# Performance work log

Measured on AMD Instinct MI355X. Metric: run time of the kernel, lower is better.

The kernel has to match this reference:

```python
import jax, jax.numpy as jnp
import numpy as np

B, PQ, C, NH, L, P, FF = 8, 900, 256, 8, 4, 4, 2048
SHAPES = [(100, 152), (50, 76), (25, 38), (13, 19)]
PK = sum(h * w for h, w in SHAPES)
DH = C // NH


def setup_inputs() -> dict:
    key = jax.random.key(0)
    ks = jax.random.split(key, 20)
    s = 0.02
    w = lambda i, shp: jax.random.normal(ks[i], shp, jnp.float32) * s
    starts = np.cumsum([0] + [h * wd for h, wd in SHAPES[:-1]]).astype(np.int64)
    return dict(
        query=w(0, (B, C, PQ)),
        key=w(1, (B, C, PK)),
        query_pos=jax.random.uniform(ks[2], (B, PQ, 3)),
        key_pos=jax.random.uniform(ks[3], (B, PK, 3)),
        reference_points=jax.random.uniform(ks[4], (B, PQ, L, 2)),
        W_in=w(5, (3 * C, C)), b_in=jnp.zeros(3 * C),
        W_out=w(6, (C, C)), b_out=jnp.zeros(C),
        W_off=w(7, (NH * L * P * 2, C)),
        b_off=jax.random.uniform(ks[8], (NH * L * P * 2,), minval=-1.0, maxval=1.0),
        W_aw=w(9, (NH * L * P, C)), b_aw=jnp.zeros(NH * L * P),
        W_v=w(10, (C, C)), b_v=jnp.zeros(C),
        W_o=w(11, (C, C)), b_o=jnp.zeros(C),
        W1=w(12, (FF, C)), b1=jnp.zeros(FF),
        W2=w(13, (C, FF)), b2=jnp.zeros(C),
        g1=jnp.ones(C), be1=jnp.zeros(C),
        g2=jnp.ones(C), be2=jnp.zeros(C),
        g3=jnp.ones(C), be3=jnp.zeros(C),
        spatial_shapes=np.array(SHAPES, np.int64),
        level_start_index=starts,
    )


def layer_norm(x, g, b):
    m = x.mean(-1, keepdims=True)
    v = x.var(-1, keepdims=True)
    return (x - m) * jax.lax.rsqrt(v + 1e-5) * g + b


def mha(x, W_in, b_in, W_out, b_out):
    # x: [S, B, C]; torch nn.MultiheadAttention with q=k=v=x
    S, Bn, _ = x.shape
    qkv = x @ W_in.T + b_in
    q, k, v = jnp.split(qkv, 3, axis=-1)
    to_h = lambda t: t.reshape(S, Bn, NH, DH).transpose(1, 2, 0, 3)  # [B,H,S,Dh]
    q, k, v = to_h(q), to_h(k), to_h(v)
    attn = jax.nn.softmax(jnp.einsum('bhqd,bhkd->bhqk', q, k) / np.sqrt(DH), axis=-1)
    o = jnp.einsum('bhqk,bhkd->bhqd', attn, v).transpose(2, 0, 1, 3).reshape(S, Bn, C)
    return o @ W_out.T + b_out


def ms_deform(value, loc, aw, shapes, starts):
    # value [B,PK,NH,DH], loc [B,PQ,NH,L,P,2] in [0,1], aw [B,PQ,NH,L,P]
    v = value.transpose(0, 2, 1, 3)          # [B,NH,PK,DH]
    locT = loc.transpose(0, 2, 1, 3, 4, 5)   # [B,NH,PQ,L,P,2]
    awT = aw.transpose(0, 2, 1, 3, 4)        # [B,NH,PQ,L,P]
    out = jnp.zeros((B, NH, PQ, DH), value.dtype)
    for l, (Hl, Wl) in enumerate(shapes):
        st = starts[l]
        vl = v[:, :, st:st + Hl * Wl]        # [B,NH,Hl*Wl,DH]
        x = locT[..., l, :, 0] * Wl - 0.5    # [B,NH,PQ,P]  (align_corners=False)
        y = locT[..., l, :, 1] * Hl - 0.5
        x0 = jnp.floor(x); y0 = jnp.floor(y)
        lw, lh = x - x0, y - y0
        x0i = x0.astype(jnp.int32); y0i = y0.astype(jnp.int32)

        def gather(ix, iy):
            valid = ((ix >= 0) & (ix < Wl) & (iy >= 0) & (iy < Hl)).astype(vl.dtype)
            idx = jnp.clip(iy, 0, Hl - 1) * Wl + jnp.clip(ix, 0, Wl - 1)
            g = jnp.take_along_axis(vl, idx.reshape(B, NH, -1, 1), axis=2)
            return g.reshape(B, NH, PQ, P, DH) * valid[..., None]

        samp = (gather(x0i, y0i) * ((1 - lw) * (1 - lh))[..., None]
                + gather(x0i + 1, y0i) * (lw * (1 - lh))[..., None]
                + gather(x0i, y0i + 1) * ((1 - lw) * lh)[..., None]
                + gather(x0i + 1, y0i + 1) * (lw * lh)[..., None])  # [B,NH,PQ,P,DH]
        out = out + (samp * awT[..., l, :, None]).sum(3)
    return out.transpose(0, 2, 1, 3).reshape(B, PQ, C)


def reference(query, key, query_pos, key_pos, reference_points,
              W_in, b_in, W_out, b_out, W_off, b_off, W_aw, b_aw,
              W_v, b_v, W_o, b_o, W1, b1, W2, b2,
              g1, be1, g2, be2, g3, be3,
              spatial_shapes, level_start_index):
    shapes = [tuple(int(t) for t in r) for r in np.asarray(spatial_shapes)]
    starts = [int(t) for t in np.asarray(level_start_index)]
    q = query.transpose(2, 0, 1)   # [PQ,B,C]
    k = key.transpose(2, 0, 1)     # [PK,B,C]
    # self-attention (posembeds are None in this config)
    q = layer_norm(q + mha(q, W_in, b_in, W_out, b_out), g1, be1)
    # multi-scale deformable cross-attention
    qd = q.transpose(1, 0, 2)      # [B,PQ,C]
    kf = k.transpose(1, 0, 2)      # [B,PK,C]
    value = (kf @ W_v.T + b_v).reshape(B, PK, NH, DH)
    off = (qd @ W_off.T + b_off).reshape(B, PQ, NH, L, P, 2)
    aw = jax.nn.softmax((qd @ W_aw.T + b_aw).reshape(B, PQ, NH, L * P), -1)
    aw = aw.reshape(B, PQ, NH, L, P)
    norm = jnp.asarray([[w_, h_] for (h_, w_) in shapes], jnp.float32)  # [L,2] as (W,H)
    loc = reference_points[:, :, None, :, None, :] + off / norm[None, None, None, :, None, :]
    q2 = ms_deform(value, loc, aw, shapes, starts) @ W_o.T + b_o
    q = layer_norm(q + q2.transpose(1, 0, 2), g2, be2)
    # FFN
    ff = jax.nn.relu(q @ W1.T + b1) @ W2.T + b2
    q = layer_norm(q + ff, g3, be3)
    return q.transpose(1, 2, 0)    # [B,C,PQ]
```

## Files before the change

kernel.cpp:

```cpp
#include <hip/hip_runtime.h>
#include <hip/hip_bf16.h>
#include <stdint.h>

typedef __hip_bfloat16 bf16;
typedef short bf16x8 __attribute__((ext_vector_type(8)));
typedef short s4v    __attribute__((ext_vector_type(4)));
typedef float f32x4  __attribute__((ext_vector_type(4)));

constexpr int B_  = 8;
constexpr int PQ_ = 900;
constexpr int C_  = 256;
constexpr int NH_ = 8;
constexpr int L_  = 4;
constexpr int P_  = 4;
constexpr int FF_ = 2048;
constexpr int DH_ = 32;
constexpr int PK_ = 20197;
constexpr int VLD = 960;

__device__ __forceinline__ short f2b(float f) {
    __hip_bfloat16 h = __float2bfloat16(f);
    union { __hip_bfloat16 h; short s; } u; u.h = h; return u.s;
}
__device__ __forceinline__ float b2f(short s) {
    union { short s; __hip_bfloat16 h; } u; u.s = s; return __bfloat162float(u.h);
}

__launch_bounds__(256)
__global__ void wcvt_kernel(const float* __restrict__ p0, const float* __restrict__ p1,
                            const float* __restrict__ p2, const float* __restrict__ p3,
                            const float* __restrict__ p4, const float* __restrict__ p5,
                            const float* __restrict__ p6, const float* __restrict__ p7,
                            short* __restrict__ dst)
{
    const int g = (blockIdx.x * 256 + threadIdx.x) * 4;
    const float* src; int off;
    if      (g < 196608)  { src = p0; off = 0; }
    else if (g < 262144)  { src = p1; off = 196608; }
    else if (g < 327680)  { src = p2; off = 262144; }
    else if (g < 360448)  { src = p3; off = 327680; }
    else if (g < 425984)  { src = p4; off = 360448; }
    else if (g < 491520)  { src = p5; off = 425984; }
    else if (g < 1015808) { src = p6; off = 491520; }
    else                  { src = p7; off = 1015808; }
    float4 v = *(const float4*)(src + (g - off));
    s4v pk = {f2b(v.x), f2b(v.y), f2b(v.z), f2b(v.w)};
    *(s4v*)&dst[g] = pk;
}

template <int NF, bool DBUF, bool AF32, bool WF32, bool CF32, bool RELU>
__launch_bounds__(256)
__global__ void mfma_gemm(const void* __restrict__ Ap, const void* __restrict__ Wp,
                          const float* __restrict__ bias, void* __restrict__ Cp,
                          int Mb, int N, int K, int tilesM,
                          int ldA, int ldW, int ldC, int nbI,
                          int64_t sAo, int64_t sAi, int64_t sWo, int64_t sWi,
                          int64_t sCo, int64_t sCi, float scale)
{
    constexpr int BN  = 64 * NF;
    constexpr int LDR = 72;
    constexpr int NB  = DBUF ? 2 : 1;
    __shared__ short As[NB * 64 * LDR];
    __shared__ short Ws[NB * BN * LDR];

    const int tid   = threadIdx.x;
    const int batch = blockIdx.y / tilesM;
    const int m0    = (blockIdx.y % tilesM) * 64;
    const int n0    = blockIdx.x * BN;
    const int outer = batch / nbI, inner = batch % nbI;
    const int64_t offA = (int64_t)outer * sAo + (int64_t)inner * sAi;
    const int64_t offW = (int64_t)outer * sWo + (int64_t)inner * sWi;
    const int64_t offC = (int64_t)outer * sCo + (int64_t)inner * sCi;

    const int w = tid >> 6, lane = tid & 63;
    const int quad = lane >> 4, lrow = lane & 15;
    const int colbase = n0 + w * 16 * NF;

    const int sm  = tid >> 2;
    const int skb = (tid & 3) * 16;

    const int T = (K + 63) / 64;

    bf16x8 areg[2];
    bf16x8 wreg[2 * NF];

    auto stageA = [&](int t) {
        const int k0 = t * 64;
        const int gm = m0 + sm;
#pragma unroll
        for (int c = 0; c < 2; ++c) {
            const int k = k0 + skb + c * 8;
            bf16x8 pk = {0, 0, 0, 0, 0, 0, 0, 0};
            if (gm < Mb && k + 8 <= K) {
                if (AF32) {
                    const float* s = (const float*)Ap + offA + (int64_t)gm * ldA + k;
                    float4 u0 = *(const float4*)s;
                    float4 u1 = *(const float4*)(s + 4);
                    pk = (bf16x8){f2b(u0.x), f2b(u0.y), f2b(u0.z), f2b(u0.w),
                                  f2b(u1.x), f2b(u1.y), f2b(u1.z), f2b(u1.w)};
                } else {
                    pk = *(const bf16x8*)((const short*)Ap + offA + (int64_t)gm * ldA + k);
                }
            }
            areg[c] = pk;
        }
    };
    auto stageW = [&](int t) {
        const int k0 = t * 64;
#pragma unroll
        for (int j = 0; j < NF; ++j) {
            const int gn = n0 + j * 64 + sm;
#pragma unroll
            for (int c = 0; c < 2; ++c) {
                const int k = k0 + skb + c * 8;
                bf16x8 pk = {0, 0, 0, 0, 0, 0, 0, 0};
                if (gn < N && k + 8 <= K) {
                    if (WF32) {
                        const float* s = (const float*)Wp + offW + (int64_t)gn * ldW + k;
                        float4 u0 = *(const float4*)s;
                        float4 u1 = *(const float4*)(s + 4);
                        pk = (bf16x8){f2b(u0.x), f2b(u0.y), f2b(u0.z), f2b(u0.w),
                                      f2b(u1.x), f2b(u1.y), f2b(u1.z), f2b(u1.w)};
                    } else {
                        pk = *(const bf16x8*)((const short*)Wp + offW + (int64_t)gn * ldW + k);
                    }
                }
                wreg[j * 2 + c] = pk;
            }
        }
    };
    auto writeLDS = [&](int buf) {
#pragma unroll
        for (int c = 0; c < 2; ++c)
            *(bf16x8*)&As[(buf * 64 + sm) * LDR + skb + c * 8] = areg[c];
#pragma unroll
        for (int j = 0; j < NF; ++j)
#pragma unroll
            for (int c = 0; c < 2; ++c)
                *(bf16x8*)&Ws[(buf * BN + j * 64 + sm) * LDR + skb + c * 8] = wreg[j * 2 + c];
    };

    f32x4 acc[4][NF];
#pragma unroll
    for (int i = 0; i < 4; ++i)
#pragma unroll
        for (int j = 0; j < NF; ++j) acc[i][j] = (f32x4){0.f, 0.f, 0.f, 0.f};

    auto compute = [&](int buf) {
        bf16x8 a[4][2], bb[NF][2];
#pragma unroll
        for (int kh = 0; kh < 2; ++kh) {
#pragma unroll
            for (int mf = 0; mf < 4; ++mf)
                a[mf][kh] = *(const bf16x8*)&As[(buf * 64 + mf * 16 + lrow) * LDR + kh * 32 + quad * 8];
#pragma unroll
            for (int nf = 0; nf < NF; ++nf)
                bb[nf][kh] = *(const bf16x8*)&Ws[(buf * BN + w * 16 * NF + nf * 16 + lrow) * LDR + kh * 32 + quad * 8];
        }
#pragma unroll
        for (int kh = 0; kh < 2; ++kh)
#pragma unroll
            for (int mf = 0; mf < 4; ++mf)
#pragma unroll
                for (int nf = 0; nf < NF; ++nf)
                    acc[mf][nf] = __builtin_amdgcn_mfma_f32_16x16x32_bf16(a[mf][kh], bb[nf][kh], acc[mf][nf], 0, 0, 0);
    };

    if (DBUF) {
        stageA(0); stageW(0); writeLDS(0);
        __syncthreads();
        for (int t = 0; t < T; ++t) {
            const int cur = t & 1;
            if (t + 1 < T) { stageA(t + 1); stageW(t + 1); }
            compute(cur);
            if (t + 1 < T) {
                writeLDS(cur ^ 1);
                __syncthreads();
            }
        }
    } else {
        for (int t = 0; t < T; ++t) {
            stageA(t); stageW(t);
            if (t > 0) __syncthreads();
            writeLDS(0);
            __syncthreads();
            compute(0);
        }
    }

#pragma unroll
    for (int nf = 0; nf < NF; ++nf) {
        const int col = colbase + nf * 16 + lrow;
        if (col >= N) continue;
        const float bia = bias ? bias[col] : 0.f;
#pragma unroll
        for (int mf = 0; mf < 4; ++mf) {
            const int row0 = m0 + mf * 16 + quad * 4;
#pragma unroll
            for (int r = 0; r < 4; ++r) {
                const int rr = row0 + r;
                if (rr < Mb) {
                    float v = acc[mf][nf][r] * scale + bia;
                    if (RELU) v = fmaxf(v, 0.f);
                    const int64_t idx = offC + (int64_t)rr * ldC + col;
                    if (CF32) ((float*)Cp)[idx] = v;
                    else      ((short*)Cp)[idx] = f2b(v);
                }
            }
        }
    }
}

template <int NF, bool DBUF, bool AF32, bool WF32, bool CF32, bool RELU>
static void mfma_launch(const void* A, const void* W, const float* bias, void* Cp,
                        int nb, int nbI, int Mb, int N, int K,
                        int ldA, int ldW, int ldC,
                        int64_t sAo, int64_t sAi, int64_t sWo, int64_t sWi,
                        int64_t sCo, int64_t sCi, float scale, hipStream_t stream)
{
    int tilesM = (Mb + 63) / 64;
    dim3 grid((N + 64 * NF - 1) / (64 * NF), nb * tilesM);
    mfma_gemm<NF, DBUF, AF32, WF32, CF32, RELU><<<grid, 256, 0, stream>>>(
        A, W, bias, Cp, Mb, N, K, tilesM, ldA, ldW, ldC, nbI,
        sAo, sAi, sWo, sWi, sCo, sCi, scale);
}

__launch_bounds__(256)
__global__ void vproj_kernel(const short* __restrict__ A, const short* __restrict__ Wb,
                             const float* __restrict__ bias, short* __restrict__ Cp,
                             int Mb, int nTiles)
{
    __shared__ short Ws[128 * 256];
    const int tid = threadIdx.x;
    const int n0 = blockIdx.x * 128;
    const int w = tid >> 6, lane = tid & 63;
    const int quad = lane >> 4, lrow = lane & 15;

    {
        const int n = tid >> 1, hk = tid & 1;
        const int64_t src = (int64_t)(n0 + n) * 256 + hk * 128;
#pragma unroll
        for (int j = 0; j < 16; ++j) {
            const int slot = hk * 16 + j;
            bf16x8 pk = *(const bf16x8*)&Wb[src + j * 8];
            *(bf16x8*)((char*)Ws + n * 512 + ((slot ^ (n & 7)) << 4)) = pk;
        }
    }
    __syncthreads();

    const int nbase = w * 32;
    float bia[2];
#pragma unroll
    for (int nf = 0; nf < 2; ++nf) bia[nf] = bias[n0 + nbase + nf * 16 + lrow];

    for (int it = 0; it < 4; ++it) {
        const int ti = blockIdx.y * 4 + it;
        if (ti >= nTiles) break;
        const int m0 = ti * 64;

        f32x4 acc[4][2];
#pragma unroll
        for (int mf = 0; mf < 4; ++mf)
#pragma unroll
            for (int nf = 0; nf < 2; ++nf) acc[mf][nf] = (f32x4){0.f, 0.f, 0.f, 0.f};

#pragma unroll
        for (int kh = 0; kh < 8; ++kh) {
            bf16x8 a[4];
#pragma unroll
            for (int mf = 0; mf < 4; ++mf) {
                const int gm = m0 + mf * 16 + lrow;
                a[mf] = (gm < Mb)
                    ? *(const bf16x8*)&A[(int64_t)gm * 256 + kh * 32 + quad * 8]
                    : (bf16x8){0, 0, 0, 0, 0, 0, 0, 0};
            }
            bf16x8 b[2];
#pragma unroll
            for (int nf = 0; nf < 2; ++nf) {
                const int n = nbase + nf * 16 + lrow;
                b[nf] = *(const bf16x8*)((const char*)Ws + n * 512 +
                                         ((((kh << 2) | quad) ^ (lrow & 7)) << 4));
            }
#pragma unroll
            for (int mf = 0; mf < 4; ++mf)
#pragma unroll
                for (int nf = 0; nf < 2; ++nf)
                    acc[mf][nf] = __builtin_amdgcn_mfma_f32_16x16x32_bf16(a[mf], b[nf], acc[mf][nf], 0, 0, 0);
        }

#pragma unroll
        for (int nf = 0; nf < 2; ++nf) {
            const int col = n0 + nbase + nf * 16 + lrow;
#pragma unroll
            for (int mf = 0; mf < 4; ++mf) {
#pragma unroll
                for (int r = 0; r < 4; ++r) {
                    const int rr = m0 + mf * 16 + quad * 4 + r;
                    if (rr < Mb)
                        Cp[(int64_t)rr * 256 + col] = f2b(acc[mf][nf][r] + bia[nf]);
                }
            }
        }
    }
}

__launch_bounds__(256)
__global__ void transpose_kernel(const float* __restrict__ src, short* __restrict__ dst,
                                 int Scount, int ldS, int64_t sbs, int64_t dbs)
{
    const int tid = threadIdx.x;
    const int b = blockIdx.z;
    const int s0 = blockIdx.x * 32, c0 = blockIdx.y * 32;
    __shared__ float t[32][33];
    {
        const int c_l = tid >> 3, sq = (tid & 7) * 4;
        const int64_t base = (int64_t)b * sbs + (int64_t)(c0 + c_l) * ldS;
#pragma unroll
        for (int i = 0; i < 4; ++i) {
            const int s = s0 + sq + i;
            t[c_l][sq + i] = (s < Scount) ? src[base + s] : 0.f;
        }
    }
    __syncthreads();
    {
        const int s_l = tid >> 3, cq = (tid & 7) * 4;
        const int s = s0 + s_l;
        if (s < Scount) {
            s4v pk = {f2b(t[cq + 0][s_l]), f2b(t[cq + 1][s_l]),
                      f2b(t[cq + 2][s_l]), f2b(t[cq + 3][s_l])};
            *(s4v*)&dst[(int64_t)b * dbs + (int64_t)s * 256 + c0 + cq] = pk;
        }
    }
}

__launch_bounds__(256)
__global__ void vt_kernel(const short* __restrict__ qkv, short* __restrict__ VT)
{
    const int tid = threadIdx.x;
    const int bh = blockIdx.y, b = bh >> 3, h = bh & 7;
    const int s0 = blockIdx.x * 32;
    __shared__ short t[32][36];
    {
        const int s_l = tid >> 3, dq = (tid & 7) * 4;
        const int s = s0 + s_l;
        s4v pk = {0, 0, 0, 0};
        if (s < 900)
            pk = *(const s4v*)&qkv[((int64_t)(b * 900 + s)) * 768 + 512 + h * 32 + dq];
        *(s4v*)&t[s_l][dq] = pk;
    }
    __syncthreads();
    {
        const int d = tid >> 3, sq = (tid & 7) * 4;
        s4v pk = {t[sq + 0][d], t[sq + 1][d], t[sq + 2][d], t[sq + 3][d]};
        *(s4v*)&VT[((int64_t)bh * 32 + d) * VLD + s0 + sq] = pk;
    }
}

__launch_bounds__(256)
__global__ void attn_fused(const short* __restrict__ qkv, const short* __restrict__ VT,
                           short* __restrict__ attno)
{
    __shared__ short Pl[4 * 16 * 72];
    const int tid = threadIdx.x;
    const int wv = tid >> 6, lane = tid & 63;
    const int quad = lane >> 4, lrow = lane & 15;
    const int bh = blockIdx.y, b = bh >> 3, h = bh & 7;
    const int q0 = blockIdx.x * 64 + wv * 16;
    const float iscale = 0.17677669529663687f;

    bf16x8 aq = {0, 0, 0, 0, 0, 0, 0, 0};
    {
        const int q = q0 + lrow;
        if (q < 900)
            aq = *(const bf16x8*)&qkv[((int64_t)(b * 900 + q)) * 768 + h * 32 + quad * 8];
    }

    float mrow[4], lsum[4];
    f32x4 o[2] = {{0.f, 0.f, 0.f, 0.f}, {0.f, 0.f, 0.f, 0.f}};
#pragma unroll
    for (int r = 0; r < 4; ++r) { mrow[r] = -1e30f; lsum[r] = 0.f; }

    short* Pw = &Pl[wv * 16 * 72];

    for (int st = 0; st < 15; ++st) {
        const int s0 = st * 64;
        f32x4 sc[4];
#pragma unroll
        for (int nf = 0; nf < 4; ++nf) {
            const int s = s0 + nf * 16 + lrow;
            bf16x8 kb = {0, 0, 0, 0, 0, 0, 0, 0};
            if (s < 900)
                kb = *(const bf16x8*)&qkv[((int64_t)(b * 900 + s)) * 768 + 256 + h * 32 + quad * 8];
            sc[nf] = __builtin_amdgcn_mfma_f32_16x16x32_bf16(aq, kb, (f32x4){0.f, 0.f, 0.f, 0.f}, 0, 0, 0);
        }
#pragma unroll
        for (int nf = 0; nf < 4; ++nf) {
            const int s = s0 + nf * 16 + lrow;
            if (s >= 900) sc[nf] = (f32x4){-1e30f, -1e30f, -1e30f, -1e30f};
            else {
#pragma unroll
                for (int r = 0; r < 4; ++r) sc[nf][r] *= iscale;
            }
        }
        float alpha[4], ps[4][4], rsum[4];
#pragma unroll
        for (int r = 0; r < 4; ++r) {
            float tm = fmaxf(fmaxf(sc[0][r], sc[1][r]), fmaxf(sc[2][r], sc[3][r]));
#pragma unroll
            for (int off = 1; off < 16; off <<= 1)
                tm = fmaxf(tm, __shfl_xor(tm, off, 64));
            const float nm = fmaxf(mrow[r], tm);
            alpha[r] = __expf(mrow[r] - nm);
            mrow[r] = nm;
            float s4 = 0.f;
#pragma unroll
            for (int nf = 0; nf < 4; ++nf) {
                const float p = __expf(sc[nf][r] - nm);
                ps[nf][r] = p;
                s4 += p;
            }
#pragma unroll
            for (int off = 1; off < 16; off <<= 1)
                s4 += __shfl_xor(s4, off, 64);
            rsum[r] = s4;
        }
#pragma unroll
        for (int nf2 = 0; nf2 < 2; ++nf2)
#pragma unroll
            for (int r = 0; r < 4; ++r) o[nf2][r] *= alpha[r];
#pragma unroll
        for (int r = 0; r < 4; ++r) lsum[r] = lsum[r] * alpha[r] + rsum[r];
#pragma unroll
        for (int nf = 0; nf < 4; ++nf)
#pragma unroll
            for (int r = 0; r < 4; ++r)
                Pw[(quad * 4 + r) * 72 + nf * 16 + lrow] = f2b(ps[nf][r]);
#pragma unroll
        for (int kh = 0; kh < 2; ++kh) {
            bf16x8 pa = *(const bf16x8*)&Pw[lrow * 72 + kh * 32 + quad * 8];
#pragma unroll
            for (int nf2 = 0; nf2 < 2; ++nf2) {
                const int d = nf2 * 16 + lrow;
                bf16x8 vb = *(const bf16x8*)&VT[((int64_t)bh * 32 + d) * VLD + s0 + kh * 32 + quad * 8];
                o[nf2] = __builtin_amdgcn_mfma_f32_16x16x32_bf16(pa, vb, o[nf2], 0, 0, 0);
            }
        }
    }
#pragma unroll
    for (int r = 0; r < 4; ++r) {
        const int q = q0 + quad * 4 + r;
        if (q < 900) {
            const float inv = 1.f / lsum[r];
#pragma unroll
            for (int nf2 = 0; nf2 < 2; ++nf2)
                attno[((int64_t)(b * 900 + q)) * 256 + h * 32 + nf2 * 16 + lrow] = f2b(o[nf2][r] * inv);
        }
    }
}

template <int MODE>
__launch_bounds__(256)
__global__ void ln_kernel(const float* __restrict__ y, const void* __restrict__ res,
                          const float* __restrict__ g, const float* __restrict__ be,
                          float* __restrict__ out_f, short* __restrict__ out_b)
{
    const int bt = blockIdx.x;
    const int b = bt / PQ_, t = bt % PQ_;
    const int c = threadIdx.x;

    float r;
    if (MODE == 0)      r = ((const float*)res)[((int64_t)b * C_ + c) * PQ_ + t];
    else if (MODE == 1) r = ((const float*)res)[(int64_t)bt * C_ + c];
    else                r = b2f(((const short*)res)[(int64_t)bt * C_ + c]);
    const float v = r + y[(int64_t)bt * C_ + c];

    __shared__ float s1[256], s2[256];
    s1[c] = v; s2[c] = v * v;
    __syncthreads();
    for (int st = 128; st > 0; st >>= 1) {
        if (c < st) { s1[c] += s1[c + st]; s2[c] += s2[c + st]; }
        __syncthreads();
    }
    const float mean = s1[0] * (1.f / C_);
    const float var  = s2[0] * (1.f / C_) - mean * mean;
    const float o = (v - mean) * rsqrtf(var + 1e-5f) * g[c] + be[c];

    if (MODE == 0) { out_f[(int64_t)bt * C_ + c] = o; out_b[(int64_t)bt * C_ + c] = f2b(o); }
    else if (MODE == 1) out_b[(int64_t)bt * C_ + c] = f2b(o);
    else out_f[((int64_t)b * C_ + c) * PQ_ + t] = o;
}

__launch_bounds__(256)
__global__ void deform_kernel(const float* __restrict__ offb, const float* __restrict__ awl,
                              const float* __restrict__ refp, const short* __restrict__ value,
                              short* __restrict__ samp)
{
    const int bt = blockIdx.x;
    const int b = bt / PQ_;
    const int tid = threadIdx.x;
    const int h = tid >> 5, d = tid & 31;

    __shared__ float Loff[256];
    __shared__ float Law[128];
    __shared__ float Lref[8];

    Loff[tid] = offb[(int64_t)bt * 256 + tid];
    if (tid < 128) Law[tid] = awl[(int64_t)bt * 128 + tid];
    if (tid < 8)   Lref[tid] = refp[(int64_t)bt * 8 + tid];
    __syncthreads();

    float m = -1e30f;
#pragma unroll
    for (int i = 0; i < 16; ++i) m = fmaxf(m, Law[h * 16 + i]);
    float s = 0.f;
#pragma unroll
    for (int i = 0; i < 16; ++i) s += __expf(Law[h * 16 + i] - m);
    const float invs = 1.f / s;

    const int HLc[4] = {100, 50, 25, 13};
    const int WLc[4] = {152, 76, 38, 19};
    const int STc[4] = {0, 15200, 19000, 19950};

    float acc = 0.f;
#pragma unroll
    for (int l = 0; l < L_; ++l) {
        const int Hl = HLc[l], Wl = WLc[l], st0 = STc[l];
        const float fx = Lref[l * 2 + 0], fy = Lref[l * 2 + 1];
#pragma unroll
        for (int p = 0; p < P_; ++p) {
            const float ox = Loff[h * 32 + l * 8 + p * 2 + 0];
            const float oy = Loff[h * 32 + l * 8 + p * 2 + 1];
            const float x = (fx + ox / (float)Wl) * (float)Wl - 0.5f;
            const float y = (fy + oy / (float)Hl) * (float)Hl - 0.5f;
            const float x0f = floorf(x), y0f = floorf(y);
            const int x0 = (int)x0f, y0 = (int)y0f;
            const float lw = x - x0f, lh = y - y0f;
            const float w00 = (1.f - lw) * (1.f - lh), w10 = lw * (1.f - lh);
            const float w01 = (1.f - lw) * lh,         w11 = lw * lh;
            const float aww = __expf(Law[h * 16 + l * 4 + p] - m) * invs;

            float sv = 0.f;
            int ix, iy; float w;
#pragma unroll
            for (int cidx = 0; cidx < 4; ++cidx) {
                if (cidx == 0) { ix = x0;     iy = y0;     w = w00; }
                if (cidx == 1) { ix = x0 + 1; iy = y0;     w = w10; }
                if (cidx == 2) { ix = x0;     iy = y0 + 1; w = w01; }
                if (cidx == 3) { ix = x0 + 1; iy = y0 + 1; w = w11; }
                if (ix >= 0 && ix < Wl && iy >= 0 && iy < Hl) {
                    const int64_t vi = ((int64_t)(b * PK_ + st0 + iy * Wl + ix)) * 256 + h * 32 + d;
                    sv += w * b2f(value[vi]);
                }
            }
            acc += sv * aww;
        }
    }
    samp[(int64_t)bt * 256 + tid] = f2b(acc);
}

extern "C" void kernel_launch(void* const* d_in, const int* in_sizes, int n_in,
                              void* d_out, int out_size, void* d_ws, size_t ws_size,
                              hipStream_t stream)
{
    const float* query = (const float*)d_in[0];
    const float* key   = (const float*)d_in[1];
    const float* refp  = (const float*)d_in[4];
    const float* W_in  = (const float*)d_in[5];
    const float* b_in  = (const float*)d_in[6];
    const float* W_out = (const float*)d_in[7];
    const float* b_out = (const float*)d_in[8];
    const float* W_off = (const float*)d_in[9];
    const float* b_off = (const float*)d_in[10];
    const float* W_aw  = (const float*)d_in[11];
    const float* b_aw  = (const float*)d_in[12];
    const float* W_v   = (const float*)d_in[13];
    const float* b_v   = (const float*)d_in[14];
    const float* W_o   = (const float*)d_in[15];
    const float* b_o   = (const float*)d_in[16];
    const float* W1    = (const float*)d_in[17];
    const float* b1    = (const float*)d_in[18];
    const float* W2    = (const float*)d_in[19];
    const float* b2    = (const float*)d_in[20];
    const float* g1    = (const float*)d_in[21];
    const float* be1   = (const float*)d_in[22];
    const float* g2    = (const float*)d_in[23];
    const float* be2   = (const float*)d_in[24];
    const float* g3    = (const float*)d_in[25];
    const float* be3   = (const float*)d_in[26];

    char* X  = (char*)d_ws;
    char* Yb = X + 62259200;
    char* Z1 = Yb + 7372800;
    char* Wa = Z1 + 7372800;
    char* Wb_ = Wa + 3686400;
    char* KT = Wb_ + 3686400;
    char* VA = KT + 82726912;
    char* WB = VA + 82726912;

    short* qkvb   = (short*)X;
    short* queryT = (short*)(X + 11059200);
    short* VT     = (short*)(X + 14745600);
    short* attno  = (short*)(X + 18677760);
    short* ffh    = (short*)X;
    float* proj   = (float*)Yb;
    float* offb   = (float*)Yb;
    float* proj2  = (float*)Yb;
    float* ffo    = (float*)Yb;
    float* q1     = (float*)Z1;
    short* q1b    = (short*)Wa;
    short* samp   = (short*)Wa;
    float* awl    = (float*)Wb_;
    short* q2nb   = (short*)Wb_;
    short* keyT   = (short*)KT;
    short* value  = (short*)VA;

    short* WBs    = (short*)WB;
    short* Wb_in  = WBs;
    short* Wb_out = WBs + 196608;
    short* Wb_off = WBs + 262144;
    short* Wb_aw  = WBs + 327680;
    short* Wb_v   = WBs + 360448;
    short* Wb_o   = WBs + 425984;
    short* Wb1    = WBs + 491520;
    short* Wb2    = WBs + 1015808;

    wcvt_kernel<<<1504, 256, 0, stream>>>(W_in, W_out, W_off, W_aw, W_v, W_o, W1, W2, WBs);
    transpose_kernel<<<dim3(29, 8, B_), 256, 0, stream>>>(query, queryT, PQ_, PQ_,
                                                          (int64_t)C_ * PQ_, (int64_t)PQ_ * C_);
    mfma_launch<1, true, false, false, false, false>(queryT, Wb_in, b_in, qkvb, 1, 1, B_ * PQ_, 768, 256,
                                                     256, 256, 768, 0, 0, 0, 0, 0, 0, 1.f, stream);
    vt_kernel<<<dim3(30, 64), 256, 0, stream>>>(qkvb, VT);
    attn_fused<<<dim3(15, 64), 256, 0, stream>>>(qkvb, VT, attno);
    mfma_launch<1, true, false, false, true, false>(attno, Wb_out, b_out, proj, 1, 1, B_ * PQ_, 256, 256,
                                                    256, 256, 256, 0, 0, 0, 0, 0, 0, 1.f, stream);
    ln_kernel<0><<<B_ * PQ_, 256, 0, stream>>>(proj, query, g1, be1, q1, q1b);
    mfma_launch<1, true, false, false, true, false>(q1b, Wb_off, b_off, offb, 1, 1, B_ * PQ_, 256, 256,
                                                    256, 256, 256, 0, 0, 0, 0, 0, 0, 1.f, stream);
    mfma_launch<1, true, false, false, true, false>(q1b, Wb_aw, b_aw, awl, 1, 1, B_ * PQ_, 128, 256,
                                                    256, 256, 128, 0, 0, 0, 0, 0, 0, 1.f, stream);
    transpose_kernel<<<dim3((PK_ + 31) / 32, 8, B_), 256, 0, stream>>>(
        key, keyT, PK_, PK_, (int64_t)C_ * PK_, (int64_t)PK_ * 256);
    {
        const int nTiles = (B_ * PK_ + 63) / 64;
        vproj_kernel<<<dim3(2, (nTiles + 3) / 4), 256, 0, stream>>>(
            keyT, Wb_v, b_v, value, B_ * PK_, nTiles);
    }
    deform_kernel<<<B_ * PQ_, 256, 0, stream>>>(offb, awl, refp, value, samp);
    mfma_launch<1, true, false, false, true, false>(samp, Wb_o, b_o, proj2, 1, 1, B_ * PQ_, 256, 256,
                                                    256, 256, 256, 0, 0, 0, 0, 0, 0, 1.f, stream);
    ln_kernel<1><<<B_ * PQ_, 256, 0, stream>>>(proj2, q1, g2, be2, nullptr, q2nb);
    mfma_launch<1, true, false, false, false, true>(q2nb, Wb1, b1, ffh, 1, 1, B_ * PQ_, FF_, 256,
                                                    256, 256, FF_, 0, 0, 0, 0, 0, 0, 1.f, stream);
    mfma_launch<1, true, false, false, true, false>(ffh, Wb2, b2, ffo, 1, 1, B_ * PQ_, 256, FF_,
                                                    FF_, FF_, 256, 0, 0, 0, 0, 0, 0, 1.f, stream);
    ln_kernel<2><<<B_ * PQ_, 256, 0, stream>>>(ffo, q2nb, g3, be3, (float*)d_out, nullptr);

    (void)in_sizes; (void)n_in; (void)out_size; (void)ws_size;
}
```

Baseline: 739.2 us.

## Hold weight tiles in registers for K=256 GEMMs and use wave-shuffle LayerNorm

Adds a GEMM kernel that loads each wave's 32-column slice of the full K=256 weight into registers once, then streams four 64-row A tiles straight from global memory into MFMA. It replaces the shared-memory vproj kernel and the generic double-buffered mfma_gemm for every K=256 projection (QKV, out-proj, offsets, attention weights, value, W_o, FFN1). The goal is to drop LDS staging and barriers and to reuse weights across row tiles. LayerNorm's tree reduction in shared memory becomes a wave shuffle reduction with a single barrier. The trade-offs are higher register pressure and uncoalesced, unstaged A loads from global memory.

```diff
diff --git a/kernel.cpp b/kernel.cpp
--- a/kernel.cpp
+++ b/kernel.cpp
@@ -46,6 +46,85 @@
     float4 v = *(const float4*)(src + (g - off));
     s4v pk = {f2b(v.x), f2b(v.y), f2b(v.z), f2b(v.w)};
     *(s4v*)&dst[g] = pk;
+}
+
+template <bool CF32, bool RELU>
+__launch_bounds__(256)
+__global__ void wreg_gemm(const short* __restrict__ A, const short* __restrict__ Wb,
+                          const float* __restrict__ bias, void* __restrict__ Cp,
+                          int Mb, int nTiles, int ldC)
+{
+    const int tid = threadIdx.x;
+    const int w = tid >> 6, lane = tid & 63;
+    const int quad = lane >> 4, lrow = lane & 15;
+    const int nbase = blockIdx.x * 128 + w * 32;
+
+    bf16x8 wreg[8][2];
+#pragma unroll
+    for (int kh = 0; kh < 8; ++kh)
+#pragma unroll
+        for (int nf = 0; nf < 2; ++nf)
+            wreg[kh][nf] = *(const bf16x8*)&Wb[(int64_t)(nbase + nf * 16 + lrow) * 256 + kh * 32 + quad * 8];
+
+    float bia[2];
+#pragma unroll
+    for (int nf = 0; nf < 2; ++nf) bia[nf] = bias ? bias[nbase + nf * 16 + lrow] : 0.f;
+
+    for (int it = 0; it < 4; ++it) {
+        const int ti = blockIdx.y * 4 + it;
+        if (ti >= nTiles) break;
+        const int m0 = ti * 64;
+
+        f32x4 acc[4][2];
+#pragma unroll
+        for (int mf = 0; mf < 4; ++mf)
+#pragma unroll
+            for (int nf = 0; nf < 2; ++nf) acc[mf][nf] = (f32x4){0.f, 0.f, 0.f, 0.f};
+
+#pragma unroll
+        for (int kh = 0; kh < 8; ++kh) {
+            bf16x8 a[4];
+#pragma unroll
+            for (int mf = 0; mf < 4; ++mf) {
+                const int gm = m0 + mf * 16 + lrow;
+                a[mf] = (gm < Mb)
+                    ? *(const bf16x8*)&A[(int64_t)gm * 256 + kh * 32 + quad * 8]
+                    : (bf16x8){0, 0, 0, 0, 0, 0, 0, 0};
+            }
+#pragma unroll
+            for (int mf = 0; mf < 4; ++mf)
+#pragma unroll
+                for (int nf = 0; nf < 2; ++nf)
+                    acc[mf][nf] = __builtin_amdgcn_mfma_f32_16x16x32_bf16(a[mf], wreg[kh][nf], acc[mf][nf], 0, 0, 0);
+        }
+
+#pragma unroll
+        for (int nf = 0; nf < 2; ++nf) {
+            const int col = nbase + nf * 16 + lrow;
+#pragma unroll
+            for (int mf = 0; mf < 4; ++mf) {
+#pragma unroll
+                for (int r = 0; r < 4; ++r) {
+                    const int rr = m0 + mf * 16 + quad * 4 + r;
+                    if (rr < Mb) {
+                        float v = acc[mf][nf][r] + bia[nf];
+                        if (RELU) v = fmaxf(v, 0.f);
+                        if (CF32) ((float*)Cp)[(int64_t)rr * ldC + col] = v;
+                        else      ((short*)Cp)[(int64_t)rr * ldC + col] = f2b(v);
+                    }
+                }
+            }
+        }
+    }
+}
+
+template <bool CF32, bool RELU>
+static void wreg_launch(const short* A, const short* Wb, const float* bias, void* Cp,
+                        int Mb, int N, int ldC, hipStream_t stream)
+{
+    const int nTiles = (Mb + 63) / 64;
+    dim3 grid(N / 128, (nTiles + 3) / 4);
+    wreg_gemm<CF32, RELU><<<grid, 256, 0, stream>>>(A, Wb, bias, Cp, Mb, nTiles, ldC);
 }
 
 template <int NF, bool DBUF, bool AF32, bool WF32, bool CF32, bool RELU>
@@ -226,85 +305,6 @@
 }
 
 __launch_bounds__(256)
-__global__ void vproj_kernel(const short* __restrict__ A, const short* __restrict__ Wb,
-                             const float* __restrict__ bias, short* __restrict__ Cp,
-                             int Mb, int nTiles)
-{
-    __shared__ short Ws[128 * 256];
-    const int tid = threadIdx.x;
-    const int n0 = blockIdx.x * 128;
-    const int w = tid >> 6, lane = tid & 63;
-    const int quad = lane >> 4, lrow = lane & 15;
-
-    {
-        const int n = tid >> 1, hk = tid & 1;
-        const int64_t src = (int64_t)(n0 + n) * 256 + hk * 128;
-#pragma unroll
-        for (int j = 0; j < 16; ++j) {
-            const int slot = hk * 16 + j;
-            bf16x8 pk = *(const bf16x8*)&Wb[src + j * 8];
-            *(bf16x8*)((char*)Ws + n * 512 + ((slot ^ (n & 7)) << 4)) = pk;
-        }
-    }
-    __syncthreads();
-
-    const int nbase = w * 32;
-    float bia[2];
-#pragma unroll
-    for (int nf = 0; nf < 2; ++nf) bia[nf] = bias[n0 + nbase + nf * 16 + lrow];
-
-    for (int it = 0; it < 4; ++it) {
-        const int ti = blockIdx.y * 4 + it;
-        if (ti >= nTiles) break;
-        const int m0 = ti * 64;
-
-        f32x4 acc[4][2];
-#pragma unroll
-        for (int mf = 0; mf < 4; ++mf)
-#pragma unroll
-            for (int nf = 0; nf < 2; ++nf) acc[mf][nf] = (f32x4){0.f, 0.f, 0.f, 0.f};
-
-#pragma unroll
-        for (int kh = 0; kh < 8; ++kh) {
-            bf16x8 a[4];
-#pragma unroll
-            for (int mf = 0; mf < 4; ++mf) {
-                const int gm = m0 + mf * 16 + lrow;
-                a[mf] = (gm < Mb)
-                    ? *(const bf16x8*)&A[(int64_t)gm * 256 + kh * 32 + quad * 8]
-                    : (bf16x8){0, 0, 0, 0, 0, 0, 0, 0};
-            }
-            bf16x8 b[2];
-#pragma unroll
-            for (int nf = 0; nf < 2; ++nf) {
-                const int n = nbase + nf * 16 + lrow;
-                b[nf] = *(const bf16x8*)((const char*)Ws + n * 512 +
-                                         ((((kh << 2) | quad) ^ (lrow & 7)) << 4));
-            }
-#pragma unroll
-            for (int mf = 0; mf < 4; ++mf)
-#pragma unroll
-                for (int nf = 0; nf < 2; ++nf)
-                    acc[mf][nf] = __builtin_amdgcn_mfma_f32_16x16x32_bf16(a[mf], b[nf], acc[mf][nf], 0, 0, 0);
-        }
-
-#pragma unroll
-        for (int nf = 0; nf < 2; ++nf) {
-            const int col = n0 + nbase + nf * 16 + lrow;
-#pragma unroll
-            for (int mf = 0; mf < 4; ++mf) {
-#pragma unroll
-                for (int r = 0; r < 4; ++r) {
-                    const int rr = m0 + mf * 16 + quad * 4 + r;
-                    if (rr < Mb)
-                        Cp[(int64_t)rr * 256 + col] = f2b(acc[mf][nf][r] + bia[nf]);
-                }
-            }
-        }
-    }
-}
-
-__launch_bounds__(256)
 __global__ void transpose_kernel(const float* __restrict__ src, short* __restrict__ dst,
                                  int Scount, int ldS, int64_t sbs, int64_t dbs)
 {
@@ -467,6 +467,7 @@
     const int bt = blockIdx.x;
     const int b = bt / PQ_, t = bt % PQ_;
     const int c = threadIdx.x;
+    const int wv = c >> 6, lane = c & 63;
 
     float r;
     if (MODE == 0)      r = ((const float*)res)[((int64_t)b * C_ + c) * PQ_ + t];
@@ -474,15 +475,19 @@
     else                r = b2f(((const short*)res)[(int64_t)bt * C_ + c]);
     const float v = r + y[(int64_t)bt * C_ + c];
 
-    __shared__ float s1[256], s2[256];
-    s1[c] = v; s2[c] = v * v;
+    __shared__ float p1[4], p2[4];
+    float a = v, sq = v * v;
+#pragma unroll
+    for (int off = 32; off > 0; off >>= 1) {
+        a  += __shfl_xor(a, off, 64);
+        sq += __shfl_xor(sq, off, 64);
+    }
+    if (lane == 0) { p1[wv] = a; p2[wv] = sq; }
     __syncthreads();
-    for (int st = 128; st > 0; st >>= 1) {
-        if (c < st) { s1[c] += s1[c + st]; s2[c] += s2[c + st]; }
-        __syncthreads();
-    }
-    const float mean = s1[0] * (1.f / C_);
-    const float var  = s2[0] * (1.f / C_) - mean * mean;
+    const float s1 = p1[0] + p1[1] + p1[2] + p1[3];
+    const float s2 = p2[0] + p2[1] + p2[2] + p2[3];
+    const float mean = s1 * (1.f / C_);
+    const float var  = s2 * (1.f / C_) - mean * mean;
     const float o = (v - mean) * rsqrtf(var + 1e-5f) * g[c] + be[c];
 
     if (MODE == 0) { out_f[(int64_t)bt * C_ + c] = o; out_b[(int64_t)bt * C_ + c] = f2b(o); }
@@ -627,30 +632,20 @@
     wcvt_kernel<<<1504, 256, 0, stream>>>(W_in, W_out, W_off, W_aw, W_v, W_o, W1, W2, WBs);
     transpose_kernel<<<dim3(29, 8, B_), 256, 0, stream>>>(query, queryT, PQ_, PQ_,
                                                           (int64_t)C_ * PQ_, (int64_t)PQ_ * C_);
-    mfma_launch<1, true, false, false, false, false>(queryT, Wb_in, b_in, qkvb, 1, 1, B_ * PQ_, 768, 256,
-                                                     256, 256, 768, 0, 0, 0, 0, 0, 0, 1.f, stream);
+    wreg_launch<false, false>(queryT, Wb_in, b_in, qkvb, B_ * PQ_, 768, 768, stream);
     vt_kernel<<<dim3(30, 64), 256, 0, stream>>>(qkvb, VT);
     attn_fused<<<dim3(15, 64), 256, 0, stream>>>(qkvb, VT, attno);
-    mfma_launch<1, true, false, false, true, false>(attno, Wb_out, b_out, proj, 1, 1, B_ * PQ_, 256, 256,
-                                                    256, 256, 256, 0, 0, 0, 0, 0, 0, 1.f, stream);
+    wreg_launch<true, false>(attno, Wb_out, b_out, proj, B_ * PQ_, 256, 256, stream);
     ln_kernel<0><<<B_ * PQ_, 256, 0, stream>>>(proj, query, g1, be1, q1, q1b);
-    mfma_launch<1, true, false, false, true, false>(q1b, Wb_off, b_off, offb, 1, 1, B_ * PQ_, 256, 256,
-                                                    256, 256, 256, 0, 0, 0, 0, 0, 0, 1.f, stream);
-    mfma_launch<1, true, false, false, true, false>(q1b, Wb_aw, b_aw, awl, 1, 1, B_ * PQ_, 128, 256,
-                                                    256, 256, 128, 0, 0, 0, 0, 0, 0, 1.f, stream);
+    wreg_launch<true, false>(q1b, Wb_off, b_off, offb, B_ * PQ_, 256, 256, stream);
+    wreg_launch<true, false>(q1b, Wb_aw, b_aw, awl, B_ * PQ_, 128, 128, stream);
     transpose_kernel<<<dim3((PK_ + 31) / 32, 8, B_), 256, 0, stream>>>(
         key, keyT, PK_, PK_, (int64_t)C_ * PK_, (int64_t)PK_ * 256);
-    {
-        const int nTiles = (B_ * PK_ + 63) / 64;
-        vproj_kernel<<<dim3(2, (nTiles + 3) / 4), 256, 0, stream>>>(
-            keyT, Wb_v, b_v, value, B_ * PK_, nTiles);
-    }
+    wreg_launch<false, false>(keyT, Wb_v, b_v, value, B_ * PK_, 256, 256, stream);
     deform_kernel<<<B_ * PQ_, 256, 0, stream>>>(offb, awl, refp, value, samp);
-    mfma_launch<1, true, false, false, true, false>(samp, Wb_o, b_o, proj2, 1, 1, B_ * PQ_, 256, 256,
-                                                    256, 256, 256, 0, 0, 0, 0, 0, 0, 1.f, stream);
+    wreg_launch<true, false>(samp, Wb_o, b_o, proj2, B_ * PQ_, 256, 256, stream);
     ln_kernel<1><<<B_ * PQ_, 256, 0, stream>>>(proj2, q1, g2, be2, nullptr, q2nb);
-    mfma_launch<1, true, false, false, false, true>(q2nb, Wb1, b1, ffh, 1, 1, B_ * PQ_, FF_, 256,
-                                                    256, 256, FF_, 0, 0, 0, 0, 0, 0, 1.f, stream);
+    wreg_launch<false, true>(q2nb, Wb1, b1, ffh, B_ * PQ_, FF_, FF_, stream);
     mfma_launch<1, true, false, false, true, false>(ffh, Wb2, b2, ffo, 1, 1, B_ * PQ_, 256, FF_,
                                                     FF_, FF_, 256, 0, 0, 0, 0, 0, 0, 1.f, stream);
     ln_kernel<2><<<B_ * PQ_, 256, 0, stream>>>(ffo, q2nb, g3, be3, (float*)d_out, nullptr);
```

Measured after the change: 804.1 us. +8.8%, slower.
